# Kernel optimization log

Hardware: AMD Instinct MI355X
Metric: run time of the kernel (lower is better)

## Reference

```python
import jax, jax.numpy as jnp
import numpy as np
from jax import lax

B, C_IN, H = 64, 3, 64
K_FEAT, KSIZE, STRIDE = 24, 8, 8
G_IN, G_HID, F_HID, OUT = 52, 256, 256, 1


def setup_inputs() -> dict:
    key = jax.random.key(0)
    ks = jax.random.split(key, 8)
    s = lambda fan_in: 1.0 / np.sqrt(fan_in)
    return {
        "image": jax.random.normal(ks[0], (B, C_IN, H, H), jnp.float32),
        "conv_w": jax.random.normal(ks[1], (K_FEAT, C_IN, KSIZE, KSIZE), jnp.float32) * s(C_IN * KSIZE * KSIZE),
        "conv_b": jnp.zeros((K_FEAT,), jnp.float32),
        "g_w1": jax.random.normal(ks[2], (G_IN, G_HID), jnp.float32) * s(G_IN),
        "g_b1": jnp.zeros((G_HID,), jnp.float32),
        "g_w2": jax.random.normal(ks[3], (G_HID, G_HID), jnp.float32) * s(G_HID),
        "g_b2": jnp.zeros((G_HID,), jnp.float32),
        "f_w1": jax.random.normal(ks[4], (G_HID, F_HID), jnp.float32) * s(G_HID),
        "f_b1": jnp.zeros((F_HID,), jnp.float32),
        "f_w2": jax.random.normal(ks[5], (F_HID, OUT), jnp.float32) * s(F_HID),
        "f_b2": jnp.zeros((OUT,), jnp.float32),
    }


def reference(image, conv_w, conv_b, g_w1, g_b1, g_w2, g_b2, f_w1, f_b1, f_w2, f_b2):
    # feature_extractor: conv k8/s8 + ReLU -> (B, k, d, d)
    x = lax.conv_general_dilated(image, conv_w, (STRIDE, STRIDE), "VALID",
                                 dimension_numbers=("NCHW", "OIHW", "NCHW"))
    x = jax.nn.relu(x + conv_b[None, :, None, None])
    b, k, d, _ = x.shape
    # coordinate channels: x varies along columns, y along rows (linspace(-1,1,d))
    coord = jnp.linspace(-1.0, 1.0, d, dtype=x.dtype)
    cx = jnp.broadcast_to(coord[None, None, None, :], (b, 1, d, d))
    cy = jnp.broadcast_to(coord[None, None, :, None], (b, 1, d, d))
    x = jnp.concatenate([x, cx, cy], axis=1)          # (B, k+2, d, d)
    k2 = k + 2
    x = x.reshape(b, k2, d * d).transpose(0, 2, 1)     # (B, d^2, k+2)
    # all-pairs: pair (i, j) -> concat(x[:, j], x[:, i])  (matches repeat/cat in torch)
    left = jnp.broadcast_to(x[:, None, :, :], (b, d * d, d * d, k2))
    right = jnp.broadcast_to(x[:, :, None, :], (b, d * d, d * d, k2))
    pairs = jnp.concatenate([left, right], axis=-1)    # (B, d^2, d^2, 2(k+2))
    # g: shared MLP over pairs
    h = jax.nn.relu(pairs @ g_w1 + g_b1)
    h = jax.nn.relu(h @ g_w2 + g_b2)                   # (B, d^2, d^2, 256)
    pooled = jnp.sum(h, axis=(1, 2))                   # sum over d^4 pairs -> (B, 256)
    # f: head MLP
    h = jax.nn.relu(pooled @ f_w1 + f_b1)
    return h @ f_w2 + f_b2                             # (B, 1)
```

## Files before the change

kernel.cpp:

```cpp
#include <hip/hip_runtime.h>
#include <hip/hip_bf16.h>
#include <stdint.h>


typedef float f32x4 __attribute__((ext_vector_type(4)));
typedef short short8 __attribute__((ext_vector_type(8)));

__device__ __forceinline__ uint32_t cvt_pk_bf16(float lo, float hi) {
    uint32_t r;
    asm("v_cvt_pk_bf16_f32 %0, %1, %2" : "=v"(r) : "v"(lo), "v"(hi));
    return r;
}

__global__ void k12_front(const float* __restrict__ img, const float* __restrict__ cw,
                          const float* __restrict__ cb, const float* __restrict__ w1,
                          const float* __restrict__ b1, const float* __restrict__ w2,
                          float* __restrict__ u, float* __restrict__ v,
                          short* __restrict__ w2f) {
    int g = blockIdx.x;
    int t = threadIdx.x;
    if (g >= 256) {
        int fi = (g - 256) * 4 + (t >> 6);
        int l = t & 63;
        int ks = fi >> 4, ni2 = fi & 15;
        int n  = ni2 * 16 + (l & 15);
        int k0 = ks * 32 + (l >> 4) * 8;
        float f[8];
        #pragma unroll
        for (int e = 0; e < 8; ++e) f[e] = w2[(k0 + e) * 256 + n];
        union { short8 s; uint32_t w[4]; } A;
        A.w[0] = cvt_pk_bf16(f[0], f[1]);
        A.w[1] = cvt_pk_bf16(f[2], f[3]);
        A.w[2] = cvt_pk_bf16(f[4], f[5]);
        A.w[3] = cvt_pk_bf16(f[6], f[7]);
        *(short8*)(w2f + (fi * 64 + l) * 8) = A.s;
        return;
    }
    __shared__ float xs[16][26];
    int b = g >> 2, q = g & 3, p0 = q * 16;

    for (int idx = t; idx < 416; idx += 256) {
        int pl = idx / 26;
        int ch = idx - pl * 26;
        int pos = p0 + pl;
        int r = pos >> 3, c = pos & 7;
        float val;
        if (ch < 24) {
            float s = cb[ch];
            #pragma unroll
            for (int ci = 0; ci < 3; ++ci)
                #pragma unroll
                for (int kr = 0; kr < 8; ++kr) {
                    const float* ip = img + ((b * 3 + ci) * 64 + r * 8 + kr) * 64 + c * 8;
                    const float* wp = cw + ((ch * 3 + ci) * 8 + kr) * 8;
                    #pragma unroll
                    for (int kc = 0; kc < 8; ++kc) s += ip[kc] * wp[kc];
                }
            val = fmaxf(s, 0.f);
        } else if (ch == 24) {
            val = -1.f + (2.f / 7.f) * (float)c;
        } else {
            val = -1.f + (2.f / 7.f) * (float)r;
        }
        xs[pl][ch] = val;
    }
    __syncthreads();

    int c = t;
    for (int r = 0; r < 16; ++r) {
        float su = b1[c], sv = 0.f;
        #pragma unroll
        for (int k = 0; k < 26; ++k) {
            float xv = xs[r][k];
            su += xv * w1[k * 256 + c];
            sv += xv * w1[(26 + k) * 256 + c];
        }
        int bj = b * 64 + p0 + r;
        u[bj * 256 + c] = su;
        v[bj * 256 + c] = sv;
    }
}

__global__ __launch_bounds__(256, 2) void k3_pairs(
        const float* __restrict__ u, const float* __restrict__ v,
        const short* __restrict__ w2f, const float* __restrict__ b2,
        float* __restrict__ part) {
    __shared__ short h1s[2][64 * 256];
    __shared__ float vs[8][256];
    int t = threadIdx.x;
    int lane = t & 63, wv = t >> 6;
    int lr = lane & 15, lg = lane >> 4;
    int blk = blockIdx.x;
    int b = blk & 63, i0 = (blk >> 6) * 8;

    {
        int q = t >> 5, c8 = (t & 31) * 8;
        const float* vr = v + (b * 64 + i0 + q) * 256 + c8;
        float4 a0 = *(const float4*)vr;
        float4 a1 = *(const float4*)(vr + 4);
        *(float4*)&vs[q][c8]     = a0;
        *(float4*)&vs[q][c8 + 4] = a1;
    }

    short8 Bf[8][4];
    #pragma unroll
    for (int ks = 0; ks < 8; ++ks)
        #pragma unroll
        for (int cg = 0; cg < 4; ++cg)
            Bf[ks][cg] = *(const short8*)(w2f + ((ks * 16 + wv * 4 + cg) * 64 + lane) * 8);

    float bias[4];
    #pragma unroll
    for (int cg = 0; cg < 4; ++cg) bias[cg] = b2[wv * 64 + cg * 16 + lr];

    const float* ub = u + b * 64 * 256;
    int kq = lane * 4;

    #define STAGE(Q, BUF)                                                          \
    {                                                                              \
        float4 vv = *(const float4*)&vs[Q][kq];                                    \
        _Pragma("unroll 4")                                                        \
        for (int rr = 0; rr < 16; ++rr) {                                          \
            int row = rr * 4 + wv;                                                 \
            float4 uu = *(const float4*)(ub + row * 256 + kq);                     \
            int2 w;                                                                \
            w.x = (int)cvt_pk_bf16(fmaxf(uu.x + vv.x, 0.f),                        \
                                   fmaxf(uu.y + vv.y, 0.f));                       \
            w.y = (int)cvt_pk_bf16(fmaxf(uu.z + vv.z, 0.f),                        \
                                   fmaxf(uu.w + vv.w, 0.f));                       \
            int byte = (row * 512 + kq * 2) ^ ((row & 7) << 4);                    \
            *(int2*)((char*)(BUF) + byte) = w;                                     \
        }                                                                          \
    }

    __syncthreads();
    STAGE(0, h1s[0])
    __syncthreads();

    float csum[4] = {0.f, 0.f, 0.f, 0.f};

    #pragma unroll 1
    for (int qq = 0; qq < 8; ++qq) {
        if (qq < 7) STAGE(qq + 1, h1s[(qq + 1) & 1])

        const char* hb = (const char*)h1s[qq & 1];
        __builtin_amdgcn_s_setprio(1);
        f32x4 acc[4][4];
        #pragma unroll
        for (int mi = 0; mi < 4; ++mi)
            #pragma unroll
            for (int cg = 0; cg < 4; ++cg) acc[mi][cg] = (f32x4){0.f, 0.f, 0.f, 0.f};

        #pragma unroll
        for (int ks = 0; ks < 8; ++ks) {
            short8 a[4];
            #pragma unroll
            for (int mi = 0; mi < 4; ++mi) {
                int row = mi * 16 + lr;
                int byte = (row * 512 + (ks * 32 + lg * 8) * 2) ^ ((row & 7) << 4);
                a[mi] = *(const short8*)(hb + byte);
            }
            #pragma unroll
            for (int cg = 0; cg < 4; ++cg)
                #pragma unroll
                for (int mi = 0; mi < 4; ++mi)
                    acc[mi][cg] = __builtin_amdgcn_mfma_f32_16x16x32_bf16(
                        a[mi], Bf[ks][cg], acc[mi][cg], 0, 0, 0);
        }
        __builtin_amdgcn_s_setprio(0);

        #pragma unroll
        for (int cg = 0; cg < 4; ++cg) {
            float s = 0.f;
            #pragma unroll
            for (int mi = 0; mi < 4; ++mi)
                #pragma unroll
                for (int r = 0; r < 4; ++r)
                    s += fmaxf(acc[mi][cg][r] + bias[cg], 0.f);
            csum[cg] += s;
        }
        __syncthreads();
    }
    #undef STAGE

    #pragma unroll
    for (int cg = 0; cg < 4; ++cg) {
        float s = csum[cg];
        s += __shfl_xor(s, 16);
        s += __shfl_xor(s, 32);
        if (lane < 16) part[blk * 256 + wv * 64 + cg * 16 + lr] = s;
    }
}

__global__ void k5_head(const float* __restrict__ part, const float* __restrict__ fw1,
                        const float* __restrict__ fb1, const float* __restrict__ fw2,
                        const float* __restrict__ fb2, float* __restrict__ out) {
    __shared__ float P[256];
    __shared__ float wsum[4];
    int b = blockIdx.x, t = threadIdx.x;
    float s0 = 0.f;
    #pragma unroll
    for (int g = 0; g < 8; ++g) s0 += part[(b + 64 * g) * 256 + t];
    P[t] = s0;
    __syncthreads();
    float s = fb1[t];
    for (int k = 0; k < 256; ++k) s += P[k] * fw1[k * 256 + t];
    float h = fmaxf(s, 0.f);
    float p = h * fw2[t];
    #pragma unroll
    for (int off = 32; off >= 1; off >>= 1) p += __shfl_xor(p, off);
    if ((t & 63) == 0) wsum[t >> 6] = p;
    __syncthreads();
    if (t == 0) out[b] = wsum[0] + wsum[1] + wsum[2] + wsum[3] + fb2[0];
}

extern "C" void kernel_launch(void* const* d_in, const int* in_sizes, int n_in,
                              void* d_out, int out_size, void* d_ws, size_t ws_size,
                              hipStream_t stream) {
    const float* image  = (const float*)d_in[0];
    const float* conv_w = (const float*)d_in[1];
    const float* conv_b = (const float*)d_in[2];
    const float* g_w1   = (const float*)d_in[3];
    const float* g_b1   = (const float*)d_in[4];
    const float* g_w2   = (const float*)d_in[5];
    const float* g_b2   = (const float*)d_in[6];
    const float* f_w1   = (const float*)d_in[7];
    const float* f_b1   = (const float*)d_in[8];
    const float* f_w2   = (const float*)d_in[9];
    const float* f_b2   = (const float*)d_in[10];
    float* out = (float*)d_out;

    char* ws = (char*)d_ws;
    float* u    = (float*)(ws + 0);
    float* v    = (float*)(ws + 4194304);
    short* w2f  = (short*)(ws + 8388608);
    float* part = (float*)(ws + 8519680);

    k12_front<<<288, 256, 0, stream>>>(image, conv_w, conv_b, g_w1, g_b1, g_w2,
                                       u, v, w2f);
    k3_pairs<<<512, 256, 0, stream>>>(u, v, w2f, g_b2, part);
    k5_head<<<64, 256, 0, stream>>>(part, f_w1, f_b1, f_w2, f_b2, out);
}
```

Measured before the change: 67.95 us.

## Interleave next-tile h1 staging with MFMA k-steps in pair kernel

The pair kernel no longer stages the next h1 tile in a separate loop before the MFMA work. Global u loads and the bf16 relu/convert/LDS store for the next tile are now spread between the eight MFMA k-steps in software-pipelined form. The v row is read straight from global memory instead of through a shared buffer, and the address swizzle is precomputed with wider 16-byte LDS writes. The epilogue and relu use packed 2-wide float math, and the head kernel splits its dot product into four independent accumulators. The interleaving raises register pressure and changes the instruction schedule, which could affect occupancy at two blocks per SM.

```diff
diff --git a/kernel.cpp b/kernel.cpp
--- a/kernel.cpp
+++ b/kernel.cpp
@@ -4,12 +4,18 @@
 
 
 typedef float f32x4 __attribute__((ext_vector_type(4)));
+typedef float f32x2 __attribute__((ext_vector_type(2)));
 typedef short short8 __attribute__((ext_vector_type(8)));
+typedef int   int4v  __attribute__((ext_vector_type(4)));
 
 __device__ __forceinline__ uint32_t cvt_pk_bf16(float lo, float hi) {
     uint32_t r;
     asm("v_cvt_pk_bf16_f32 %0, %1, %2" : "=v"(r) : "v"(lo), "v"(hi));
     return r;
+}
+__device__ __forceinline__ f32x2 relu2(f32x2 a) {
+    f32x2 z = (f32x2){0.f, 0.f};
+    return __builtin_elementwise_max(a, z);
 }
 
 __global__ void k12_front(const float* __restrict__ img, const float* __restrict__ cw,
@@ -81,27 +87,50 @@
     }
 }
 
+#define ULOAD(P, X0, X1)                                          \
+    { X0 = *(const f32x4*)(uth + (P) * 2048);                     \
+      X1 = *(const f32x4*)(uth + (P) * 2048 + 4); }
+
+#define CONSUME(P, X0, X1, VA, VB, WB)                            \
+    { f32x2 a0 = relu2((f32x2){X0.x, X0.y} + (f32x2){VA.x, VA.y});\
+      f32x2 a1 = relu2((f32x2){X0.z, X0.w} + (f32x2){VA.z, VA.w});\
+      f32x2 a2 = relu2((f32x2){X1.x, X1.y} + (f32x2){VB.x, VB.y});\
+      f32x2 a3 = relu2((f32x2){X1.z, X1.w} + (f32x2){VB.z, VB.w});\
+      int4v d;                                                    \
+      d.x = (int)cvt_pk_bf16(a0.x, a0.y);                         \
+      d.y = (int)cvt_pk_bf16(a1.x, a1.y);                         \
+      d.z = (int)cvt_pk_bf16(a2.x, a2.y);                         \
+      d.w = (int)cvt_pk_bf16(a3.x, a3.y);                         \
+      *(int4v*)((WB) + (P) * 4096) = d; }
+
+#define MFMA_ROW(AV, MI, KS)                                                           \
+      acc[MI][0] = __builtin_amdgcn_mfma_f32_16x16x32_bf16(AV, Bf[KS][0], acc[MI][0], 0, 0, 0); \
+      acc[MI][1] = __builtin_amdgcn_mfma_f32_16x16x32_bf16(AV, Bf[KS][1], acc[MI][1], 0, 0, 0); \
+      acc[MI][2] = __builtin_amdgcn_mfma_f32_16x16x32_bf16(AV, Bf[KS][2], acc[MI][2], 0, 0, 0); \
+      acc[MI][3] = __builtin_amdgcn_mfma_f32_16x16x32_bf16(AV, Bf[KS][3], acc[MI][3], 0, 0, 0);
+
+#define MFMA_KS(KS)                                                   \
+    { const char* hx = ((KS) & 1) ? hO : hE;                          \
+      short8 a0 = *(const short8*)(hx + ((KS) >> 1) * 128);           \
+      short8 a1 = *(const short8*)(hx + 8192  + ((KS) >> 1) * 128);   \
+      short8 a2 = *(const short8*)(hx + 16384 + ((KS) >> 1) * 128);   \
+      short8 a3 = *(const short8*)(hx + 24576 + ((KS) >> 1) * 128);   \
+      __builtin_amdgcn_s_setprio(1);                                  \
+      MFMA_ROW(a0, 0, KS) MFMA_ROW(a1, 1, KS)                         \
+      MFMA_ROW(a2, 2, KS) MFMA_ROW(a3, 3, KS)                         \
+      __builtin_amdgcn_s_setprio(0); }
+
 __global__ __launch_bounds__(256, 2) void k3_pairs(
         const float* __restrict__ u, const float* __restrict__ v,
         const short* __restrict__ w2f, const float* __restrict__ b2,
         float* __restrict__ part) {
     __shared__ short h1s[2][64 * 256];
-    __shared__ float vs[8][256];
     int t = threadIdx.x;
     int lane = t & 63, wv = t >> 6;
     int lr = lane & 15, lg = lane >> 4;
     int blk = blockIdx.x;
     int b = blk & 63, i0 = (blk >> 6) * 8;
 
-    {
-        int q = t >> 5, c8 = (t & 31) * 8;
-        const float* vr = v + (b * 64 + i0 + q) * 256 + c8;
-        float4 a0 = *(const float4*)vr;
-        float4 a1 = *(const float4*)(vr + 4);
-        *(float4*)&vs[q][c8]     = a0;
-        *(float4*)&vs[q][c8 + 4] = a1;
-    }
-
     short8 Bf[8][4];
     #pragma unroll
     for (int ks = 0; ks < 8; ++ks)
@@ -109,83 +138,88 @@
         for (int cg = 0; cg < 4; ++cg)
             Bf[ks][cg] = *(const short8*)(w2f + ((ks * 16 + wv * 4 + cg) * 64 + lane) * 8);
 
-    float bias[4];
-    #pragma unroll
-    for (int cg = 0; cg < 4; ++cg) bias[cg] = b2[wv * 64 + cg * 16 + lr];
-
-    const float* ub = u + b * 64 * 256;
-    int kq = lane * 4;
-
-    #define STAGE(Q, BUF)                                                          \
-    {                                                                              \
-        float4 vv = *(const float4*)&vs[Q][kq];                                    \
-        _Pragma("unroll 4")                                                        \
-        for (int rr = 0; rr < 16; ++rr) {                                          \
-            int row = rr * 4 + wv;                                                 \
-            float4 uu = *(const float4*)(ub + row * 256 + kq);                     \
-            int2 w;                                                                \
-            w.x = (int)cvt_pk_bf16(fmaxf(uu.x + vv.x, 0.f),                        \
-                                   fmaxf(uu.y + vv.y, 0.f));                       \
-            w.y = (int)cvt_pk_bf16(fmaxf(uu.z + vv.z, 0.f),                        \
-                                   fmaxf(uu.w + vv.w, 0.f));                       \
-            int byte = (row * 512 + kq * 2) ^ ((row & 7) << 4);                    \
-            *(int2*)((char*)(BUF) + byte) = w;                                     \
-        }                                                                          \
-    }
-
-    __syncthreads();
-    STAGE(0, h1s[0])
-    __syncthreads();
-
-    float csum[4] = {0.f, 0.f, 0.f, 0.f};
+    f32x2 bias2[4];
+    #pragma unroll
+    for (int cg = 0; cg < 4; ++cg) {
+        float bv = b2[wv * 64 + cg * 16 + lr];
+        bias2[cg] = (f32x2){bv, bv};
+    }
+
+    int col16 = t & 31, rowbase = t >> 5;
+    const float* uth = u + (b * 64 + rowbase) * 256 + col16 * 8;
+    const float* vth = v + (b * 64 + i0) * 256 + col16 * 8;
+    int wbase = rowbase * 512 + ((col16 * 16) ^ (rowbase << 4));
+
+    int xb = (lg * 16) ^ ((lr & 7) << 4);
+    int rE = lr * 512 + xb;
+    int rO = lr * 512 + (xb ^ 64);
+
+    {
+        f32x4 va = *(const f32x4*)(vth);
+        f32x4 vb = *(const f32x4*)(vth + 4);
+        char* wb0 = (char*)h1s[0] + wbase;
+        f32x4 x0, x1;
+        #pragma unroll
+        for (int p = 0; p < 8; ++p) {
+            ULOAD(p, x0, x1)
+            CONSUME(p, x0, x1, va, vb, wb0)
+        }
+    }
+    __syncthreads();
+
+    f32x2 csum2[4];
+    #pragma unroll
+    for (int cg = 0; cg < 4; ++cg) csum2[cg] = (f32x2){0.f, 0.f};
+    const float* vnp = vth + 256;
 
     #pragma unroll 1
     for (int qq = 0; qq < 8; ++qq) {
-        if (qq < 7) STAGE(qq + 1, h1s[(qq + 1) & 1])
-
-        const char* hb = (const char*)h1s[qq & 1];
-        __builtin_amdgcn_s_setprio(1);
+        const char* hE = (const char*)h1s[qq & 1] + rE;
+        const char* hO = (const char*)h1s[qq & 1] + rO;
+        char* wb = (char*)h1s[(qq & 1) ^ 1] + wbase;
+        bool pre = (qq < 7);
+
         f32x4 acc[4][4];
         #pragma unroll
         for (int mi = 0; mi < 4; ++mi)
             #pragma unroll
             for (int cg = 0; cg < 4; ++cg) acc[mi][cg] = (f32x4){0.f, 0.f, 0.f, 0.f};
 
-        #pragma unroll
-        for (int ks = 0; ks < 8; ++ks) {
-            short8 a[4];
+        f32x4 va, vb, x0, x1, y0, y1;
+        if (pre) { va = *(const f32x4*)vnp; vb = *(const f32x4*)(vnp + 4); ULOAD(0, x0, x1) }
+        MFMA_KS(0)
+        if (pre) { ULOAD(1, y0, y1) CONSUME(0, x0, x1, va, vb, wb) }
+        MFMA_KS(1)
+        if (pre) { ULOAD(2, x0, x1) CONSUME(1, y0, y1, va, vb, wb) }
+        MFMA_KS(2)
+        if (pre) { ULOAD(3, y0, y1) CONSUME(2, x0, x1, va, vb, wb) }
+        MFMA_KS(3)
+        if (pre) { ULOAD(4, x0, x1) CONSUME(3, y0, y1, va, vb, wb) }
+        MFMA_KS(4)
+        if (pre) { ULOAD(5, y0, y1) CONSUME(4, x0, x1, va, vb, wb) }
+        MFMA_KS(5)
+        if (pre) { ULOAD(6, x0, x1) CONSUME(5, y0, y1, va, vb, wb) }
+        MFMA_KS(6)
+        if (pre) { ULOAD(7, y0, y1) CONSUME(6, x0, x1, va, vb, wb) }
+        MFMA_KS(7)
+        if (pre) { CONSUME(7, y0, y1, va, vb, wb) }
+
+        #pragma unroll
+        for (int cg = 0; cg < 4; ++cg) {
             #pragma unroll
             for (int mi = 0; mi < 4; ++mi) {
-                int row = mi * 16 + lr;
-                int byte = (row * 512 + (ks * 32 + lg * 8) * 2) ^ ((row & 7) << 4);
-                a[mi] = *(const short8*)(hb + byte);
+                f32x2 lo = relu2((f32x2){acc[mi][cg].x, acc[mi][cg].y} + bias2[cg]);
+                f32x2 hi = relu2((f32x2){acc[mi][cg].z, acc[mi][cg].w} + bias2[cg]);
+                csum2[cg] = csum2[cg] + lo + hi;
             }
-            #pragma unroll
-            for (int cg = 0; cg < 4; ++cg)
-                #pragma unroll
-                for (int mi = 0; mi < 4; ++mi)
-                    acc[mi][cg] = __builtin_amdgcn_mfma_f32_16x16x32_bf16(
-                        a[mi], Bf[ks][cg], acc[mi][cg], 0, 0, 0);
-        }
-        __builtin_amdgcn_s_setprio(0);
-
-        #pragma unroll
-        for (int cg = 0; cg < 4; ++cg) {
-            float s = 0.f;
-            #pragma unroll
-            for (int mi = 0; mi < 4; ++mi)
-                #pragma unroll
-                for (int r = 0; r < 4; ++r)
-                    s += fmaxf(acc[mi][cg][r] + bias[cg], 0.f);
-            csum[cg] += s;
         }
         __syncthreads();
-    }
-    #undef STAGE
+        vnp += 256;
+    }
 
     #pragma unroll
     for (int cg = 0; cg < 4; ++cg) {
-        float s = csum[cg];
+        float s = csum2[cg].x + csum2[cg].y;
         s += __shfl_xor(s, 16);
         s += __shfl_xor(s, 32);
         if (lane < 16) part[blk * 256 + wv * 64 + cg * 16 + lr] = s;
@@ -203,9 +237,14 @@
     for (int g = 0; g < 8; ++g) s0 += part[(b + 64 * g) * 256 + t];
     P[t] = s0;
     __syncthreads();
-    float s = fb1[t];
-    for (int k = 0; k < 256; ++k) s += P[k] * fw1[k * 256 + t];
-    float h = fmaxf(s, 0.f);
+    float a0 = 0.f, a1 = 0.f, a2 = 0.f, a3 = 0.f;
+    for (int k = 0; k < 64; ++k) {
+        a0 += P[k]       * fw1[k * 256 + t];
+        a1 += P[k + 64]  * fw1[(k + 64) * 256 + t];
+        a2 += P[k + 128] * fw1[(k + 128) * 256 + t];
+        a3 += P[k + 192] * fw1[(k + 192) * 256 + t];
+    }
+    float h = fmaxf(fb1[t] + a0 + a1 + a2 + a3, 0.f);
     float p = h * fw2[t];
     #pragma unroll
     for (int off = 32; off >= 1; off >>= 1) p += __shfl_xor(p, off);
```

Measured after the change: 83.51 us. 1.23x slower.
